# Kernel tuning notes

Measured on AMD Instinct MI355X. Metric: run time of the kernel, lower is better.

Reference implementation:

```python
import jax, jax.numpy as jnp
import numpy as np

K = 1024
D = 64
BETA = 0.25


def setup_inputs() -> dict:
    key = jax.random.key(0)
    k1, k2 = jax.random.split(key)
    x = jax.random.normal(k1, (32, D, 64, 64), dtype=jnp.float32)
    # torch init: uniform(-1/K, 1/K)
    emb = jax.random.uniform(k2, (K, D), dtype=jnp.float32, minval=-1.0 / K, maxval=1.0 / K)
    return {"x": x, "emb": emb}


def reference(x, emb):
    B, C, H, W = x.shape
    z = jnp.transpose(x, (0, 2, 3, 1))          # [B,H,W,D]
    zf = z.reshape(-1, C)                        # [N,D]
    # squared euclidean distances ||z||^2 + ||e||^2 - 2 z.e
    dist = (jnp.sum(zf * zf, axis=1, keepdims=True)
            + jnp.sum(emb * emb, axis=1)
            - 2.0 * jnp.matmul(zf, emb.T))       # [N,K]
    min_idx = jnp.argmin(dist, axis=1)           # [N]
    # one-hot @ emb == gather
    z_q = emb[min_idx].reshape(z.shape)          # [B,H,W,D]
    sg = jax.lax.stop_gradient
    embedding_loss = (jnp.mean((sg(z_q) - z) ** 2)
                      + BETA * jnp.mean((z_q - sg(z)) ** 2))
    z_q_st = z + sg(z_q - z)                     # straight-through
    # code-usage perplexity
    n = zf.shape[0]
    e_mean = jnp.bincount(min_idx, length=K).astype(z.dtype) / n
    perplexity = jnp.exp(-jnp.sum(e_mean * jnp.log(e_mean + 1e-10)))
    z_q_out = jnp.transpose(z_q_st, (0, 3, 1, 2))  # [B,D,H,W]
    return embedding_loss, z_q_out, perplexity
```

## Files before the change

### kernel.cpp

```cpp
#include <hip/hip_runtime.h>
#include <math.h>

#define D_    64
#define K_    1024
#define N_    131072
#define HW_   4096
#define TAU   4e-5f
#define NKT   64

typedef unsigned long long ull;
typedef unsigned short ushort;
typedef short  bf16x8  __attribute__((ext_vector_type(8)));
typedef float  f32x4   __attribute__((ext_vector_type(4)));
typedef ushort ushort8 __attribute__((ext_vector_type(8)));

__device__ __forceinline__ ushort f2bf(float f) {
    unsigned u = __float_as_uint(f);
    return (ushort)((u + 0x7FFFu + ((u >> 16) & 1u)) >> 16);
}
__device__ __forceinline__ float b2f(ushort h) {
    return __uint_as_float((unsigned)h << 16);
}
#define SLOT(seg, code) ((seg) * 16 + ((code) ^ (seg)))

__device__ __forceinline__ void block_sync_lds() {
    asm volatile("s_waitcnt lgkmcnt(0)" ::: "memory");
    __builtin_amdgcn_s_barrier();
}

__global__ __launch_bounds__(256)
void vq_prep(const float* __restrict__ emb, ushort* __restrict__ ehg,
             ushort* __restrict__ elg, float* __restrict__ e2g,
             float* __restrict__ embT, int* __restrict__ hist,
             int* __restrict__ cnt, double* __restrict__ ssqd) {
    const int n = blockIdx.x * 256 + threadIdx.x;
    if (n < K_) {
        const float* er = emb + (size_t)n * D_;
        float e2 = 0.0f;
        #pragma unroll
        for (int d8 = 0; d8 < 8; ++d8) {
            ushort8 hh, ll;
            #pragma unroll
            for (int j = 0; j < 8; ++j) {
                float e = er[d8 * 8 + j];
                e2 = fmaf(e, e, e2);
                ushort h = f2bf(e);
                hh[j] = h;
                ll[j] = f2bf(e - b2f(h));
                embT[(size_t)(d8 * 8 + j) * K_ + n] = e;
            }
            *(ushort8*)(ehg + (size_t)n * D_ + d8 * 8) = hh;
            *(ushort8*)(elg + (size_t)n * D_ + d8 * 8) = ll;
        }
        e2g[n] = e2;
        hist[n] = 0;
    }
    if (n == 0 && blockIdx.x == 0) { *cnt = 0; *ssqd = 0.0; }
}

#define STEP(CUR, S, PF)                                                      \
    {                                                                         \
        const bf16x8 bh0 = *(const bf16x8*)(&bst[CUR][0][SLOT(g,     c16)][0]); \
        const bf16x8 bh1 = *(const bf16x8*)(&bst[CUR][0][SLOT(g + 4, c16)][0]); \
        const bf16x8 bl0 = *(const bf16x8*)(&bst[CUR][1][SLOT(g,     c16)][0]); \
        const bf16x8 bl1 = *(const bf16x8*)(&bst[CUR][1][SLOT(g + 4, c16)][0]); \
        const int   c_  = (S) * 16 + c16;                                     \
        const float E2  = e2g[c_];                                            \
        f32x4 ac[4];                                                          \
        _Pragma("unroll")                                                     \
        for (int t = 0; t < 4; ++t) {                                         \
            f32x4 a = {0.0f, 0.0f, 0.0f, 0.0f};                               \
            a = __builtin_amdgcn_mfma_f32_16x16x32_bf16(ah[t][0], bh0, a, 0, 0, 0); \
            a = __builtin_amdgcn_mfma_f32_16x16x32_bf16(al[t][0], bh0, a, 0, 0, 0); \
            a = __builtin_amdgcn_mfma_f32_16x16x32_bf16(ah[t][1], bh1, a, 0, 0, 0); \
            a = __builtin_amdgcn_mfma_f32_16x16x32_bf16(al[t][1], bh1, a, 0, 0, 0); \
            a = __builtin_amdgcn_mfma_f32_16x16x32_bf16(ah[t][0], bl0, a, 0, 0, 0); \
            a = __builtin_amdgcn_mfma_f32_16x16x32_bf16(ah[t][1], bl1, a, 0, 0, 0); \
            ac[t] = a;                                                        \
        }                                                                     \
         \
        _Pragma("unroll")                                                     \
        for (int t = 0; t < 4; ++t) {                                         \
            _Pragma("unroll")                                                 \
            for (int q = 0; q < 4; ++q) {                                     \
                float dist = fmaf(-2.0f, ac[t][q], E2);                       \
                const int st = t * 4 + q;                                     \
                float vmax = fmaxf(dist, v1[st]);                             \
                bool lt = dist < v1[st];                                      \
                k1[st] = lt ? c_ : k1[st];                                    \
                v1[st] = fminf(dist, v1[st]);                                 \
                v2[st] = fminf(v2[st], vmax);                                 \
            }                                                                 \
        }                                                                     \
        if ((S) + 1 < NKT)                                                    \
            *(ushort8*)(&bst[(CUR) ^ 1][sHalf][sSlot][0]) = PF;               \
        if ((S) + 3 < NKT)                                                    \
            PF = *(const ushort8*)(sBase + (size_t)((S) + 3) * 16 * D_);      \
        block_sync_lds();                                                     \
    }

__global__ __launch_bounds__(256, 2)
void vq_mfma(const float* __restrict__ x, const float* __restrict__ emb,
             const ushort* __restrict__ ehg, const ushort* __restrict__ elg,
             const float* __restrict__ e2g, float* __restrict__ zq_out,
             int* __restrict__ list, int* __restrict__ cnt,
             int* __restrict__ hist, double* __restrict__ ssqd) {
    __shared__ ushort bst[2][2][128][8];
    __shared__ int lkfin[256];

    const int tid = threadIdx.x;
    const int wv  = tid >> 6;
    const int l   = tid & 63;
    const int g   = l >> 4;
    const int c16 = l & 15;
    const int n0b = blockIdx.x * 256;
    const int n0w = n0b + wv * 64;

    const int sHalf = tid >> 7;
    const int sS    = tid & 127;
    const int sCode = sS >> 3;
    const int sSeg  = sS & 7;
    const int sSlot = SLOT(sSeg, sCode);
    const ushort* sBase = (sHalf ? elg : ehg) + (size_t)sCode * D_ + sSeg * 8;

    bf16x8 ah[4][2], al[4][2];
    #pragma unroll
    for (int t = 0; t < 4; ++t) {
        const int row = n0w + t * 16 + c16;
        const int b = row >> 12, hw = row & (HW_ - 1);
        const float* xr = x + (size_t)b * (D_ * HW_) + hw;
        #pragma unroll
        for (int s = 0; s < 2; ++s) {
            #pragma unroll
            for (int j = 0; j < 8; ++j) {
                float z = xr[(size_t)(g * 8 + s * 32 + j) * HW_];
                ushort h = f2bf(z);
                ah[t][s][j] = (short)h;
                al[t][s][j] = (short)f2bf(z - b2f(h));
            }
        }
    }

    float v1[16], v2[16]; int k1[16];
    #pragma unroll
    for (int st = 0; st < 16; ++st) { v1[st] = 3.4e38f; v2[st] = 3.4e38f; k1[st] = 0; }

    *(ushort8*)(&bst[0][sHalf][sSlot][0]) = *(const ushort8*)(sBase);
    ushort8 pf0 = *(const ushort8*)(sBase + (size_t)1 * 16 * D_);
    ushort8 pf1 = *(const ushort8*)(sBase + (size_t)2 * 16 * D_);
    __syncthreads();

    #pragma unroll 1
    for (int s = 0; s < NKT; s += 2) {
        STEP(0, s,     pf0)
        STEP(1, s + 1, pf1)
    }

    #pragma unroll
    for (int off = 1; off < 16; off <<= 1) {
        #pragma unroll
        for (int st = 0; st < 16; ++st) {
            float w1 = __shfl_xor(v1[st], off, 64);
            float w2 = __shfl_xor(v2[st], off, 64);
            int   wk = __shfl_xor(k1[st], off, 64);
            float lose = (w1 < v1[st]) ? v1[st] : w1;
            v2[st] = fminf(fminf(v2[st], w2), lose);
            if (w1 < v1[st]) { v1[st] = w1; k1[st] = wk; }
        }
    }

    if (c16 == 0) {
        #pragma unroll
        for (int t = 0; t < 4; ++t) {
            #pragma unroll
            for (int q = 0; q < 4; ++q) {
                const int st = t * 4 + q;
                const int rr = wv * 64 + t * 16 + 4 * g + q;
                int kk;
                if (!(v2[st] - v1[st] > TAU)) {
                    int i = atomicAdd(cnt, 1);
                    list[i] = n0b + rr;
                    kk = -1;
                } else {
                    kk = k1[st];
                    atomicAdd(&hist[kk], 1);
                }
                lkfin[rr] = kk;
            }
        }
    }
    __syncthreads();

    const int n  = n0b + tid;
    const int b2_ = n >> 12, hw2 = n & (HW_ - 1);
    const float* xr2  = x      + (size_t)b2_ * (D_ * HW_) + hw2;
    float*       outr = zq_out + (size_t)b2_ * (D_ * HW_) + hw2;
    const int kk = lkfin[tid];
    float ls = 0.0f;
    if (kk >= 0) {
        const float* er = emb + (size_t)kk * D_;
        #pragma unroll
        for (int d = 0; d < D_; ++d) {
            float zv = xr2[(size_t)d * HW_];
            float t  = er[d] - zv;
            ls = fmaf(t, t, ls);
            outr[(size_t)d * HW_] = zv + t;
        }
    }
    #pragma unroll
    for (int o = 32; o > 0; o >>= 1) ls += __shfl_down(ls, o, 64);
    if (l == 0) atomicAdd(ssqd, (double)ls);
}

__global__ __launch_bounds__(256)
void vq_exact(const float* __restrict__ x, const float* __restrict__ emb,
              const float* __restrict__ embT, const float* __restrict__ e2g,
              const int* __restrict__ list, const int* __restrict__ cnt,
              float* __restrict__ zq_out, int* __restrict__ hist,
              double* __restrict__ ssqd) {
    const int l  = threadIdx.x & 63;
    const int gw = (blockIdx.x * 256 + threadIdx.x) >> 6;
    const int nw = (gridDim.x * 256) >> 6;
    const int C  = *cnt;
    for (int i = gw; i < C; i += nw) {
        const int n = list[i];
        const int b = n >> 12, hw = n & (HW_ - 1);
        const float* xr = x + (size_t)b * (D_ * HW_) + hw;
        const float zval = xr[(size_t)l * HW_];
        float r2 = 0.0f;
        float s[16];
        #pragma unroll
        for (int j = 0; j < 16; ++j) s[j] = 0.0f;
        for (int d = 0; d < D_; ++d) {
            const float zd = __shfl(zval, d, 64);
            r2 = fmaf(zd, zd, r2);
            const float* erow = embT + (size_t)d * K_ + l * 4;
            const float4 e0 = *(const float4*)(erow);
            const float4 e1 = *(const float4*)(erow + 256);
            const float4 e2 = *(const float4*)(erow + 512);
            const float4 e3 = *(const float4*)(erow + 768);
            s[0]  = fmaf(zd, e0.x, s[0]);  s[1]  = fmaf(zd, e0.y, s[1]);
            s[2]  = fmaf(zd, e0.z, s[2]);  s[3]  = fmaf(zd, e0.w, s[3]);
            s[4]  = fmaf(zd, e1.x, s[4]);  s[5]  = fmaf(zd, e1.y, s[5]);
            s[6]  = fmaf(zd, e1.z, s[6]);  s[7]  = fmaf(zd, e1.w, s[7]);
            s[8]  = fmaf(zd, e2.x, s[8]);  s[9]  = fmaf(zd, e2.y, s[9]);
            s[10] = fmaf(zd, e2.z, s[10]); s[11] = fmaf(zd, e2.w, s[11]);
            s[12] = fmaf(zd, e3.x, s[12]); s[13] = fmaf(zd, e3.y, s[13]);
            s[14] = fmaf(zd, e3.z, s[14]); s[15] = fmaf(zd, e3.w, s[15]);
        }
        ull best = ~0ull;
        #pragma unroll
        for (int j = 0; j < 16; ++j) {
            const int k = (j >> 2) * 256 + l * 4 + (j & 3);
            float dist = fmaf(-2.0f, s[j], r2 + e2g[k]);
            ull p = ((ull)__float_as_uint(dist) << 32) | (unsigned)k;
            if (p < best) best = p;
        }
        #pragma unroll
        for (int off = 1; off < 64; off <<= 1) {
            ull q = __shfl_xor(best, off, 64);
            if (q < best) best = q;
        }
        const int k = (int)(best & 0xffffffffull);
        const float e = emb[(size_t)k * D_ + l];
        const float t = e - zval;
        float ps = t * t;
        float* outr = zq_out + (size_t)b * (D_ * HW_) + hw;
        outr[(size_t)l * HW_] = zval + t;
        #pragma unroll
        for (int off = 32; off > 0; off >>= 1) ps += __shfl_down(ps, off, 64);
        if (l == 0) {
            atomicAdd(&hist[k], 1);
            atomicAdd(ssqd, (double)ps);
        }
    }
}

__global__ __launch_bounds__(1024)
void vq_final(const int* __restrict__ hist, const double* __restrict__ ssqd,
              float* __restrict__ out_loss, float* __restrict__ out_perp) {
    __shared__ float wred[16];
    int t = threadIdx.x;
    float cnt = (float)hist[t];
    float em  = cnt / (float)N_;
    float s   = em * logf(em + 1e-10f);
    #pragma unroll
    for (int o = 32; o > 0; o >>= 1) s += __shfl_down(s, o, 64);
    if ((t & 63) == 0) wred[t >> 6] = s;
    __syncthreads();
    if (t == 0) {
        float tot = 0.0f;
        for (int w = 0; w < 16; ++w) tot += wred[w];
        *out_perp = expf(-tot);
        float mse = (float)(*ssqd / (double)((size_t)N_ * D_));
        *out_loss = mse + 0.25f * mse;
    }
}

extern "C" void kernel_launch(void* const* d_in, const int* in_sizes, int n_in,
                              void* d_out, int out_size, void* d_ws, size_t ws_size,
                              hipStream_t stream) {
    const float* x   = (const float*)d_in[0];
    const float* emb = (const float*)d_in[1];
    float* out  = (float*)d_out;
    float* loss = out;
    float* zq   = out + 1;
    float* perp = out + 1 + (size_t)N_ * D_;

    char* w = (char*)d_ws;
    int*    list = (int*)w;     w += (size_t)N_ * 4;
    ushort* ehg  = (ushort*)w;  w += (size_t)K_ * D_ * 2;
    ushort* elg  = (ushort*)w;  w += (size_t)K_ * D_ * 2;
    float*  embT = (float*)w;   w += (size_t)K_ * D_ * 4;
    float*  e2g  = (float*)w;   w += (size_t)K_ * 4;
    int*    hist = (int*)w;     w += (size_t)K_ * 4;
    int*    cnt  = (int*)w;     w += 16;
    double* ssqd = (double*)w;

    vq_prep<<<dim3(4), dim3(256), 0, stream>>>(emb, ehg, elg, e2g, embT, hist, cnt, ssqd);
    vq_mfma<<<dim3(N_ / 256), dim3(256), 0, stream>>>(x, emb, ehg, elg, e2g, zq, list, cnt, hist, ssqd);
    vq_exact<<<dim3(2048), dim3(256), 0, stream>>>(x, emb, embT, e2g, list, cnt, zq, hist, ssqd);
    vq_final<<<dim3(1), dim3(1024), 0, stream>>>(hist, ssqd, loss, perp);
}
```

Baseline: 148.2 us.

## Stage codebook tiles per wave to drop block-wide barriers; prioritize MFMA issue

Each wave now loads and double-buffers its own copy of the codebook hi/lo bf16 tiles in a private LDS slice. That removes the block-wide s_barrier and lgkmcnt wait after every 16-code step, relying on in-order LDS access within a wave instead. It also raises wave priority around the MFMA sequence with s_setprio. The cost is four times the global/L2 reads and LDS writes for the codebook, plus four times the LDS footprint for staging.

Measured after the change: 157.3 us. 6.1% more time.

```diff
diff --git a/kernel.cpp b/kernel.cpp
--- a/kernel.cpp
+++ b/kernel.cpp
@@ -22,11 +22,6 @@
     return __uint_as_float((unsigned)h << 16);
 }
 #define SLOT(seg, code) ((seg) * 16 + ((code) ^ (seg)))
-
-__device__ __forceinline__ void block_sync_lds() {
-    asm volatile("s_waitcnt lgkmcnt(0)" ::: "memory");
-    __builtin_amdgcn_s_barrier();
-}
 
 __global__ __launch_bounds__(256)
 void vq_prep(const float* __restrict__ emb, ushort* __restrict__ ehg,
@@ -58,15 +53,16 @@
     if (n == 0 && blockIdx.x == 0) { *cnt = 0; *ssqd = 0.0; }
 }
 
-#define STEP(CUR, S, PF)                                                      \
+#define STEP(CUR, S, PH0, PH1, PL0, PL1)                                      \
     {                                                                         \
-        const bf16x8 bh0 = *(const bf16x8*)(&bst[CUR][0][SLOT(g,     c16)][0]); \
-        const bf16x8 bh1 = *(const bf16x8*)(&bst[CUR][0][SLOT(g + 4, c16)][0]); \
-        const bf16x8 bl0 = *(const bf16x8*)(&bst[CUR][1][SLOT(g,     c16)][0]); \
-        const bf16x8 bl1 = *(const bf16x8*)(&bst[CUR][1][SLOT(g + 4, c16)][0]); \
+        const bf16x8 bh0 = *(const bf16x8*)(&bst[wv][CUR][0][SLOT(g,     c16)][0]); \
+        const bf16x8 bh1 = *(const bf16x8*)(&bst[wv][CUR][0][SLOT(g + 4, c16)][0]); \
+        const bf16x8 bl0 = *(const bf16x8*)(&bst[wv][CUR][1][SLOT(g,     c16)][0]); \
+        const bf16x8 bl1 = *(const bf16x8*)(&bst[wv][CUR][1][SLOT(g + 4, c16)][0]); \
         const int   c_  = (S) * 16 + c16;                                     \
         const float E2  = e2g[c_];                                            \
         f32x4 ac[4];                                                          \
+        __builtin_amdgcn_s_setprio(1);                                        \
         _Pragma("unroll")                                                     \
         for (int t = 0; t < 4; ++t) {                                         \
             f32x4 a = {0.0f, 0.0f, 0.0f, 0.0f};                               \
@@ -78,6 +74,7 @@
             a = __builtin_amdgcn_mfma_f32_16x16x32_bf16(ah[t][1], bl1, a, 0, 0, 0); \
             ac[t] = a;                                                        \
         }                                                                     \
+        __builtin_amdgcn_s_setprio(0);                                        \
          \
         _Pragma("unroll")                                                     \
         for (int t = 0; t < 4; ++t) {                                         \
@@ -92,11 +89,19 @@
                 v2[st] = fminf(v2[st], vmax);                                 \
             }                                                                 \
         }                                                                     \
-        if ((S) + 1 < NKT)                                                    \
-            *(ushort8*)(&bst[(CUR) ^ 1][sHalf][sSlot][0]) = PF;               \
-        if ((S) + 3 < NKT)                                                    \
-            PF = *(const ushort8*)(sBase + (size_t)((S) + 3) * 16 * D_);      \
-        block_sync_lds();                                                     \
+        if ((S) + 1 < NKT) {                                                  \
+            *(ushort8*)(&bst[wv][(CUR) ^ 1][0][slot0][0]) = PH0;              \
+            *(ushort8*)(&bst[wv][(CUR) ^ 1][0][slot1][0]) = PH1;              \
+            *(ushort8*)(&bst[wv][(CUR) ^ 1][1][slot0][0]) = PL0;              \
+            *(ushort8*)(&bst[wv][(CUR) ^ 1][1][slot1][0]) = PL1;              \
+        }                                                                     \
+        if ((S) + 3 < NKT) {                                                  \
+            const size_t o_ = (size_t)((S) + 3) * 1024;                       \
+            PH0 = *(const ushort8*)(hsrc + o_);                               \
+            PH1 = *(const ushort8*)(hsrc + o_ + 8);                           \
+            PL0 = *(const ushort8*)(lsrc + o_);                               \
+            PL1 = *(const ushort8*)(lsrc + o_ + 8);                           \
+        }                                                                     \
     }
 
 __global__ __launch_bounds__(256, 2)
@@ -105,7 +110,7 @@
              const float* __restrict__ e2g, float* __restrict__ zq_out,
              int* __restrict__ list, int* __restrict__ cnt,
              int* __restrict__ hist, double* __restrict__ ssqd) {
-    __shared__ ushort bst[2][2][128][8];
+    __shared__ ushort bst[4][2][2][128][8];
     __shared__ int lkfin[256];
 
     const int tid = threadIdx.x;
@@ -116,12 +121,12 @@
     const int n0b = blockIdx.x * 256;
     const int n0w = n0b + wv * 64;
 
-    const int sHalf = tid >> 7;
-    const int sS    = tid & 127;
-    const int sCode = sS >> 3;
-    const int sSeg  = sS & 7;
-    const int sSlot = SLOT(sSeg, sCode);
-    const ushort* sBase = (sHalf ? elg : ehg) + (size_t)sCode * D_ + sSeg * 8;
+    const int sCode = l >> 2;
+    const int sSeg0 = (l & 3) * 2;
+    const int slot0 = SLOT(sSeg0,     sCode);
+    const int slot1 = SLOT(sSeg0 + 1, sCode);
+    const ushort* hsrc = ehg + (size_t)l * 16;
+    const ushort* lsrc = elg + (size_t)l * 16;
 
     bf16x8 ah[4][2], al[4][2];
     #pragma unroll
@@ -145,15 +150,29 @@
     #pragma unroll
     for (int st = 0; st < 16; ++st) { v1[st] = 3.4e38f; v2[st] = 3.4e38f; k1[st] = 0; }
 
-    *(ushort8*)(&bst[0][sHalf][sSlot][0]) = *(const ushort8*)(sBase);
-    ushort8 pf0 = *(const ushort8*)(sBase + (size_t)1 * 16 * D_);
-    ushort8 pf1 = *(const ushort8*)(sBase + (size_t)2 * 16 * D_);
-    __syncthreads();
+    {
+        ushort8 h0 = *(const ushort8*)(hsrc);
+        ushort8 h1 = *(const ushort8*)(hsrc + 8);
+        ushort8 l0 = *(const ushort8*)(lsrc);
+        ushort8 l1 = *(const ushort8*)(lsrc + 8);
+        *(ushort8*)(&bst[wv][0][0][slot0][0]) = h0;
+        *(ushort8*)(&bst[wv][0][0][slot1][0]) = h1;
+        *(ushort8*)(&bst[wv][0][1][slot0][0]) = l0;
+        *(ushort8*)(&bst[wv][0][1][slot1][0]) = l1;
+    }
+    ushort8 ph0 = *(const ushort8*)(hsrc + 1024);
+    ushort8 ph1 = *(const ushort8*)(hsrc + 1024 + 8);
+    ushort8 pl0 = *(const ushort8*)(lsrc + 1024);
+    ushort8 pl1 = *(const ushort8*)(lsrc + 1024 + 8);
+    ushort8 qh0 = *(const ushort8*)(hsrc + 2048);
+    ushort8 qh1 = *(const ushort8*)(hsrc + 2048 + 8);
+    ushort8 ql0 = *(const ushort8*)(lsrc + 2048);
+    ushort8 ql1 = *(const ushort8*)(lsrc + 2048 + 8);
 
     #pragma unroll 1
     for (int s = 0; s < NKT; s += 2) {
-        STEP(0, s,     pf0)
-        STEP(1, s + 1, pf1)
+        STEP(0, s,     ph0, ph1, pl0, pl1)
+        STEP(1, s + 1, qh0, qh1, ql0, ql1)
     }
 
     #pragma unroll
```
